# Kernel tuning notes

Hardware: AMD Instinct MI355X
Metric: run time of the kernel (lower is better)

## Reference

```python
import jax, jax.numpy as jnp
import numpy as np

EPS = 1e-7
TWO_PI = 2.0 * np.pi

K = 4096   # num gaussians
R = 8192   # num rays
MAP_SIZE = 100


def setup_inputs() -> dict:
    key = jax.random.key(0)
    k1, k2, k3, k4, k5, k6 = jax.random.split(key, 6)
    pos_raw = jax.random.normal(k1, (K, 2), dtype=jnp.float32)            # pre-sigmoid positions
    conc_raw = jax.random.normal(k2, (K,), dtype=jnp.float32)             # pre-softplus concentration
    scale_raw = 0.1 * jax.random.normal(k3, (K, 2), dtype=jnp.float32)    # log-scales
    rot_raw = jax.random.uniform(k4, (K,), dtype=jnp.float32) * TWO_PI    # rotation angles
    p_rays = jax.random.uniform(k5, (R, 2), dtype=jnp.float32) * MAP_SIZE # ray origins in map coords
    u = jax.random.normal(k6, (R, 2), dtype=jnp.float32)
    u_rays = u / jnp.linalg.norm(u, axis=-1, keepdims=True)               # unit ray directions
    return {"pos_raw": pos_raw, "conc_raw": conc_raw, "scale_raw": scale_raw,
            "rot_raw": rot_raw, "p_rays": p_rays, "u_rays": u_rays,
            "map_size": MAP_SIZE}


def _forward(pos_raw, conc_raw, scale_raw, rot_raw, p_rays, u_rays, map_size):
    # --- per-gaussian activations (GasSplattingModel getters) ---
    pos = jax.nn.sigmoid(pos_raw) * map_size           # (K,2)
    conc = jax.nn.softplus(conc_raw)                   # (K,)
    scale = jnp.exp(scale_raw)                         # (K,2)
    d0 = 1.0 / (scale[:, 0] ** 2 + EPS)                # diag of S^2 inverse
    d1 = 1.0 / (scale[:, 1] ** 2 + EPS)
    c, s = jnp.cos(rot_raw), jnp.sin(rot_raw)
    # Sigma^{-1} = R diag(d0,d1) R^T with R = [[c,-s],[s,c]]  (symmetric 2x2)
    m00 = c * c * d0 + s * s * d1                      # (K,)
    m01 = c * s * (d0 - d1)
    m11 = s * s * d0 + c * c * d1
    M = jnp.stack([m00, m01, m11], axis=0)             # (3,K) quadratic-form coeffs

    u0, u1 = u_rays[:, 0], u_rays[:, 1]
    p0, p1 = p_rays[:, 0], p_rays[:, 1]

    # quadratic-form features per ray, contracted with M via GEMM -> (R,K)
    qu = jnp.stack([u0 * u0, 2.0 * u0 * u1, u1 * u1], axis=1)        # (R,3)
    qp = jnp.stack([p0 * p0, 2.0 * p0 * p1, p1 * p1], axis=1)        # (R,3)
    qup = jnp.stack([u0 * p0, u0 * p1 + u1 * p0, u1 * p1], axis=1)   # (R,3)
    a = qu @ M          # u^T S u      (R,K)
    pSp = qp @ M        # p^T S p      (R,K)
    uSp = qup @ M       # u^T S p      (R,K)

    # S @ mu per gaussian -> (2,K)
    Sm = jnp.stack([m00 * pos[:, 0] + m01 * pos[:, 1],
                    m01 * pos[:, 0] + m11 * pos[:, 1]], axis=0)
    uSm = u_rays @ Sm   # u^T S mu     (R,K)
    pSm = p_rays @ Sm   # p^T S mu     (R,K)
    mSm = pos[:, 0] * Sm[0] + pos[:, 1] * Sm[1]        # mu^T S mu (K,)

    b = uSp - uSm                                      # u^T S (p - mu)
    c0 = pSp - 2.0 * pSm + mSm[None, :]                # (p-mu)^T S (p-mu)

    # closed-form line integral of conc * exp(-0.5 (x-mu)^T S (x-mu)) along ray
    dens = conc[None, :] * jnp.sqrt(TWO_PI / a) * jnp.exp(-0.5 * (c0 - b * b / a))
    return jnp.sum(dens, axis=-1)                      # (R,)


def reference(pos_raw, conc_raw, scale_raw, rot_raw, p_rays, u_rays, map_size):
    return _forward(pos_raw, conc_raw, scale_raw, rot_raw, p_rays, u_rays, map_size)
```

## Files before the change

kernel.cpp:

```cpp
#include <hip/hip_runtime.h>
#include <hip/hip_bf16.h>

#define EPS 1e-07f

#define BLOCK 256
#define SLICE 64

#define SQRT_HALF_LOG2E 0.84932180028801904f
#define LOG2_SQRT_2PI   1.32574806473616588f

typedef float v4f __attribute__((ext_vector_type(4)));

__global__ void precompute_gauss(const float* __restrict__ pos_raw,
                                 const float* __restrict__ conc_raw,
                                 const float* __restrict__ scale_raw,
                                 const float* __restrict__ rot_raw,
                                 const void*  __restrict__ map_size_p,
                                 float* __restrict__ gF,
                                 float* __restrict__ out,
                                 int K, int R)
{
    int k = blockIdx.x * blockDim.x + threadIdx.x;
    int nthreads = gridDim.x * blockDim.x;

    for (int i = k; i < R; i += nthreads) out[i] = 0.0f;

    if (k >= K) return;

    unsigned int msbits = *(const unsigned int*)map_size_p;
    float msf = __uint_as_float(msbits);
    float ms;
    if (msf >= 1e-3f && msf <= 1e9f) ms = msf;
    else                             ms = (float)(*(const int*)map_size_p);

    float pr0 = pos_raw[2*k],  pr1 = pos_raw[2*k+1];
    float pos0 = ms / (1.0f + expf(-pr0));
    float pos1 = ms / (1.0f + expf(-pr1));

    float cr = conc_raw[k];
    float conc = fmaxf(cr, 0.0f) + log1pf(expf(-fabsf(cr)));

    float s0 = expf(scale_raw[2*k]);
    float s1 = expf(scale_raw[2*k+1]);
    float d0 = 1.0f / (s0*s0 + EPS);
    float d1 = 1.0f / (s1*s1 + EPS);

    float rot = rot_raw[k];
    float c = cosf(rot), s = sinf(rot);

    float m00 = c*c*d0 + s*s*d1;
    float m01 = c*s*(d0 - d1);
    float m11 = s*s*d0 + c*c*d1;

    float det    = d0 * d1;
    float invdet = 1.0f / det;

    float cc = log2f(conc) + LOG2_SQRT_2PI - 0.5f * log2f(det);

    gF[0*K + k] = m00 * invdet;
    gF[1*K + k] = m01 * invdet;
    gF[2*K + k] = m11 * invdet;
    gF[3*K + k] = cc;
    gF[4*K + k] = pos0;
    gF[5*K + k] = pos1;
}

__global__ __launch_bounds__(BLOCK) void splat_main(
        const float* __restrict__ p_rays,
        const float* __restrict__ u_rays,
        const float* __restrict__ gF,
        float* __restrict__ out,
        int K)
{
    __shared__ float sF[6][SLICE];

    const int ray = blockIdx.x * BLOCK + threadIdx.x;
    const int k0  = blockIdx.y * SLICE;
    const int nk  = min(SLICE, K - k0);

    for (int i = threadIdx.x; i < 6*SLICE; i += BLOCK) {
        int f = i >> 6;
        int c = i & (SLICE - 1);
        if (c < nk) sF[f][c] = gF[f*K + k0 + c];
    }
    __syncthreads();

    float2 p2 = *(const float2*)(p_rays + 2*ray);
    float2 u2 = *(const float2*)(u_rays + 2*ray);
    const float p0 = p2.x, p1 = p2.y;
    const float u0 = u2.x, u1 = u2.y;

    const float qu0 = u0*u0, qu1 = 2.0f*u0*u1, qu2 = u1*u1;

    const float wt   =  SQRT_HALF_LOG2E * (u0*p1 - u1*p0);
    const float ut1  =  SQRT_HALF_LOG2E * u1;
    const float nut0 = -SQRT_HALF_LOG2E * u0;

    float acc = 0.0f;

    const int nk4 = nk & ~3;
    for (int t4 = 0; t4 < nk4; t4 += 4) {
        v4f M00 = *(const v4f*)&sF[0][t4];
        v4f M01 = *(const v4f*)&sF[1][t4];
        v4f M11 = *(const v4f*)&sF[2][t4];
        v4f CC  = *(const v4f*)&sF[3][t4];
        v4f P0  = *(const v4f*)&sF[4][t4];
        v4f P1  = *(const v4f*)&sF[5][t4];

        #pragma unroll
        for (int g = 0; g < 4; ++g) {
            float a  = fmaf(qu2, M11[g], fmaf(qu1, M01[g], qu0 * M00[g]));
            float cr = fmaf(nut0, P1[g], fmaf(ut1, P0[g], wt));
            float ra = __builtin_amdgcn_rsqf(a);
            float t  = cr * ra;
            float ar = fmaf(-t, t, CC[g]);
            float e  = __builtin_amdgcn_exp2f(ar);
            acc = fmaf(ra, e, acc);
        }
    }
    for (int j = nk4; j < nk; ++j) {
        float a  = fmaf(qu2, sF[2][j], fmaf(qu1, sF[1][j], qu0 * sF[0][j]));
        float cr = fmaf(nut0, sF[5][j], fmaf(ut1, sF[4][j], wt));
        float ra = __builtin_amdgcn_rsqf(a);
        float t  = cr * ra;
        float ar = fmaf(-t, t, sF[3][j]);
        float e  = __builtin_amdgcn_exp2f(ar);
        acc = fmaf(ra, e, acc);
    }

    atomicAdd(&out[ray], acc);
}

extern "C" void kernel_launch(void* const* d_in, const int* in_sizes, int n_in,
                              void* d_out, int out_size, void* d_ws, size_t ws_size,
                              hipStream_t stream)
{
    const float* pos_raw   = (const float*)d_in[0];
    const float* conc_raw  = (const float*)d_in[1];
    const float* scale_raw = (const float*)d_in[2];
    const float* rot_raw   = (const float*)d_in[3];
    const float* p_rays    = (const float*)d_in[4];
    const float* u_rays    = (const float*)d_in[5];
    const void*  map_size  = d_in[6];

    const int K = in_sizes[1];
    const int R = out_size;

    float* out = (float*)d_out;
    float* gF  = (float*)d_ws;

    {
        dim3 grid((K + BLOCK - 1) / BLOCK);
        precompute_gauss<<<grid, BLOCK, 0, stream>>>(pos_raw, conc_raw, scale_raw,
                                                     rot_raw, map_size,
                                                     gF, out, K, R);
    }
    {
        dim3 grid(R / BLOCK, (K + SLICE - 1) / SLICE);
        splat_main<<<grid, BLOCK, 0, stream>>>(p_rays, u_rays, gF, out, K);
    }
}
```

Measured before the change: 21.42 us.

## Fuse gaussian precompute into splat kernel with in-block ray reduction

Merges the per-gaussian activation precompute into the main splat kernel. Each 1024-thread block handles 32 rays and recomputes all gaussian parameters into shared memory in two halves, then splits the gaussian range across 32 lane groups and reduces partial sums through a shuffle and shared memory. This removes the second launch, the workspace round trip, the zeroing of the output and the global atomics. In exchange, every one of the 256 blocks redoes the full transcendental precompute for all K gaussians with fast-math intrinsics. Only 256 blocks are launched, and the code assumes K is divisible by 256.

Result: no change. 21.03 us (-1.8%).

```diff
diff --git a/kernel.cpp b/kernel.cpp
--- a/kernel.cpp
+++ b/kernel.cpp
@@ -3,132 +3,134 @@
 
 #define EPS 1e-07f
 
-#define BLOCK 256
-#define SLICE 64
+#define BLOCK 1024
+#define RPB   32
+#define NW    (BLOCK/64)
 
 #define SQRT_HALF_LOG2E 0.84932180028801904f
 #define LOG2_SQRT_2PI   1.32574806473616588f
 
 typedef float v4f __attribute__((ext_vector_type(4)));
 
-__global__ void precompute_gauss(const float* __restrict__ pos_raw,
-                                 const float* __restrict__ conc_raw,
-                                 const float* __restrict__ scale_raw,
-                                 const float* __restrict__ rot_raw,
-                                 const void*  __restrict__ map_size_p,
-                                 float* __restrict__ gF,
-                                 float* __restrict__ out,
-                                 int K, int R)
+__global__ __launch_bounds__(BLOCK) void fused_splat(
+        const float* __restrict__ pos_raw,
+        const float* __restrict__ conc_raw,
+        const float* __restrict__ scale_raw,
+        const float* __restrict__ rot_raw,
+        const void*  __restrict__ map_size_p,
+        const float* __restrict__ p_rays,
+        const float* __restrict__ u_rays,
+        float* __restrict__ out,
+        int K, int R)
 {
-    int k = blockIdx.x * blockDim.x + threadIdx.x;
-    int nthreads = gridDim.x * blockDim.x;
+    __shared__ float sG[512][6][4];
+    __shared__ float psum[NW][RPB];
 
-    for (int i = k; i < R; i += nthreads) out[i] = 0.0f;
+    const int tid  = threadIdx.x;
+    const int lane = tid & 63;
+    const int wv   = tid >> 6;
+    const int rayl = lane & 31;
+    const int half = lane >> 5;
+    const int chunk = (wv << 1) | half;
 
-    if (k >= K) return;
+    int ray = blockIdx.x * RPB + rayl;
+    if (ray >= R) ray = R - 1;
 
     unsigned int msbits = *(const unsigned int*)map_size_p;
     float msf = __uint_as_float(msbits);
-    float ms;
-    if (msf >= 1e-3f && msf <= 1e9f) ms = msf;
-    else                             ms = (float)(*(const int*)map_size_p);
-
-    float pr0 = pos_raw[2*k],  pr1 = pos_raw[2*k+1];
-    float pos0 = ms / (1.0f + expf(-pr0));
-    float pos1 = ms / (1.0f + expf(-pr1));
-
-    float cr = conc_raw[k];
-    float conc = fmaxf(cr, 0.0f) + log1pf(expf(-fabsf(cr)));
-
-    float s0 = expf(scale_raw[2*k]);
-    float s1 = expf(scale_raw[2*k+1]);
-    float d0 = 1.0f / (s0*s0 + EPS);
-    float d1 = 1.0f / (s1*s1 + EPS);
-
-    float rot = rot_raw[k];
-    float c = cosf(rot), s = sinf(rot);
-
-    float m00 = c*c*d0 + s*s*d1;
-    float m01 = c*s*(d0 - d1);
-    float m11 = s*s*d0 + c*c*d1;
-
-    float det    = d0 * d1;
-    float invdet = 1.0f / det;
-
-    float cc = log2f(conc) + LOG2_SQRT_2PI - 0.5f * log2f(det);
-
-    gF[0*K + k] = m00 * invdet;
-    gF[1*K + k] = m01 * invdet;
-    gF[2*K + k] = m11 * invdet;
-    gF[3*K + k] = cc;
-    gF[4*K + k] = pos0;
-    gF[5*K + k] = pos1;
-}
-
-__global__ __launch_bounds__(BLOCK) void splat_main(
-        const float* __restrict__ p_rays,
-        const float* __restrict__ u_rays,
-        const float* __restrict__ gF,
-        float* __restrict__ out,
-        int K)
-{
-    __shared__ float sF[6][SLICE];
-
-    const int ray = blockIdx.x * BLOCK + threadIdx.x;
-    const int k0  = blockIdx.y * SLICE;
-    const int nk  = min(SLICE, K - k0);
-
-    for (int i = threadIdx.x; i < 6*SLICE; i += BLOCK) {
-        int f = i >> 6;
-        int c = i & (SLICE - 1);
-        if (c < nk) sF[f][c] = gF[f*K + k0 + c];
-    }
-    __syncthreads();
+    const float ms = (msf >= 1e-3f && msf <= 1e9f) ? msf
+                                                   : (float)(*(const int*)map_size_p);
 
     float2 p2 = *(const float2*)(p_rays + 2*ray);
     float2 u2 = *(const float2*)(u_rays + 2*ray);
-    const float p0 = p2.x, p1 = p2.y;
-    const float u0 = u2.x, u1 = u2.y;
-
-    const float qu0 = u0*u0, qu1 = 2.0f*u0*u1, qu2 = u1*u1;
-
+    const float p0 = p2.x, p1 = p2.y, u0 = u2.x, u1 = u2.y;
+    const float qu0  = u0*u0, qu1 = 2.0f*u0*u1, qu2 = u1*u1;
     const float wt   =  SQRT_HALF_LOG2E * (u0*p1 - u1*p0);
-    const float ut1  =  SQRT_HALF_LOG2E * u1;
-    const float nut0 = -SQRT_HALF_LOG2E * u0;
+    const float su1  =  SQRT_HALF_LOG2E * u1;
+    const float nsu0 = -SQRT_HALF_LOG2E * u0;
 
     float acc = 0.0f;
 
-    const int nk4 = nk & ~3;
-    for (int t4 = 0; t4 < nk4; t4 += 4) {
-        v4f M00 = *(const v4f*)&sF[0][t4];
-        v4f M01 = *(const v4f*)&sF[1][t4];
-        v4f M11 = *(const v4f*)&sF[2][t4];
-        v4f CC  = *(const v4f*)&sF[3][t4];
-        v4f P0  = *(const v4f*)&sF[4][t4];
-        v4f P1  = *(const v4f*)&sF[5][t4];
+    const int KH = K >> 1;
+    const int CL = KH >> 5;
+    const int NG = CL >> 2;
 
-        #pragma unroll
-        for (int g = 0; g < 4; ++g) {
-            float a  = fmaf(qu2, M11[g], fmaf(qu1, M01[g], qu0 * M00[g]));
-            float cr = fmaf(nut0, P1[g], fmaf(ut1, P0[g], wt));
-            float ra = __builtin_amdgcn_rsqf(a);
-            float t  = cr * ra;
-            float ar = fmaf(-t, t, CC[g]);
-            float e  = __builtin_amdgcn_exp2f(ar);
-            acc = fmaf(ra, e, acc);
+    for (int pass = 0; pass < 2; ++pass) {
+        const int kbase = pass * KH;
+
+        __syncthreads();
+
+        for (int k = tid; k < KH; k += BLOCK) {
+            const int kg = kbase + k;
+
+            float pr0 = pos_raw[2*kg], pr1 = pos_raw[2*kg+1];
+            float pos0 = ms / (1.0f + __expf(-pr0));
+            float pos1 = ms / (1.0f + __expf(-pr1));
+
+            float cr = conc_raw[kg];
+            float conc = fmaxf(cr, 0.0f) + __logf(1.0f + __expf(-fabsf(cr)));
+
+            float s0 = __expf(scale_raw[2*kg]);
+            float s1 = __expf(scale_raw[2*kg+1]);
+            float d0 = 1.0f / (s0*s0 + EPS);
+            float d1 = 1.0f / (s1*s1 + EPS);
+
+            float rot = rot_raw[kg];
+            float c = __cosf(rot), s = __sinf(rot);
+
+            float m00 = c*c*d0 + s*s*d1;
+            float m01 = c*s*(d0 - d1);
+            float m11 = s*s*d0 + c*c*d1;
+
+            float det    = d0 * d1;
+            float invdet = 1.0f / det;
+            float cc = __log2f(conc) + LOG2_SQRT_2PI - 0.5f * __log2f(det);
+
+            const int q = k >> 2, e = k & 3;
+            sG[q][0][e] = m00 * invdet;
+            sG[q][1][e] = m01 * invdet;
+            sG[q][2][e] = m11 * invdet;
+            sG[q][3][e] = cc;
+            sG[q][4][e] = pos0;
+            sG[q][5][e] = pos1;
+        }
+        __syncthreads();
+
+        const int g0 = chunk * NG;
+        #pragma unroll 4
+        for (int gq = 0; gq < NG; ++gq) {
+            const int t4 = g0 + gq;
+            v4f M00 = *(const v4f*)&sG[t4][0][0];
+            v4f M01 = *(const v4f*)&sG[t4][1][0];
+            v4f M11 = *(const v4f*)&sG[t4][2][0];
+            v4f CC  = *(const v4f*)&sG[t4][3][0];
+            v4f P0  = *(const v4f*)&sG[t4][4][0];
+            v4f P1  = *(const v4f*)&sG[t4][5][0];
+
+            #pragma unroll
+            for (int g = 0; g < 4; ++g) {
+                float a_  = fmaf(qu2, M11[g], fmaf(qu1, M01[g], qu0 * M00[g]));
+                float cr_ = fmaf(nsu0, P1[g], fmaf(su1, P0[g], wt));
+                float ra_ = __builtin_amdgcn_rsqf(a_);
+                float t_  = cr_ * ra_;
+                float ar_ = fmaf(-t_, t_, CC[g]);
+                float e_  = __builtin_amdgcn_exp2f(ar_);
+                acc = fmaf(ra_, e_, acc);
+            }
         }
     }
-    for (int j = nk4; j < nk; ++j) {
-        float a  = fmaf(qu2, sF[2][j], fmaf(qu1, sF[1][j], qu0 * sF[0][j]));
-        float cr = fmaf(nut0, sF[5][j], fmaf(ut1, sF[4][j], wt));
-        float ra = __builtin_amdgcn_rsqf(a);
-        float t  = cr * ra;
-        float ar = fmaf(-t, t, sF[3][j]);
-        float e  = __builtin_amdgcn_exp2f(ar);
-        acc = fmaf(ra, e, acc);
+
+    acc += __shfl_xor(acc, 32, 64);
+    if (half == 0) psum[wv][rayl] = acc;
+    __syncthreads();
+
+    if (wv == 0 && lane < RPB) {
+        float s = 0.0f;
+        #pragma unroll
+        for (int w = 0; w < NW; ++w) s += psum[w][lane];
+        int oray = blockIdx.x * RPB + lane;
+        if (oray < R) out[oray] = s;
     }
-
-    atomicAdd(&out[ray], acc);
 }
 
 extern "C" void kernel_launch(void* const* d_in, const int* in_sizes, int n_in,
@@ -147,16 +149,9 @@
     const int R = out_size;
 
     float* out = (float*)d_out;
-    float* gF  = (float*)d_ws;
 
-    {
-        dim3 grid((K + BLOCK - 1) / BLOCK);
-        precompute_gauss<<<grid, BLOCK, 0, stream>>>(pos_raw, conc_raw, scale_raw,
-                                                     rot_raw, map_size,
-                                                     gF, out, K, R);
-    }
-    {
-        dim3 grid(R / BLOCK, (K + SLICE - 1) / SLICE);
-        splat_main<<<grid, BLOCK, 0, stream>>>(p_rays, u_rays, gF, out, K);
-    }
+    dim3 grid((R + RPB - 1) / RPB);
+    fused_splat<<<grid, BLOCK, 0, stream>>>(pos_raw, conc_raw, scale_raw,
+                                            rot_raw, map_size,
+                                            p_rays, u_rays, out, K, R);
 }
```
